# Kernel tuning notes

Hardware: AMD Instinct MI355X
Metric: run time of the kernel (lower is better)

The kernel has to match this reference:

```python
import jax, jax.numpy as jnp
import numpy as np

N_NODES = 50000
N_EDGES = 600000
D_IN = 128
D_OUT = 128


def mean_propagate(x, edge_index, num_nodes):
    # edge_index[0] = source nodes, edge_index[1] = destination nodes
    src, dst = edge_index[0], edge_index[1]
    gathered = x[src]                                   # [E, D]
    summed = jax.ops.segment_sum(gathered, dst, num_segments=num_nodes)  # [N, D]
    deg = jax.ops.segment_sum(jnp.ones((edge_index.shape[1],), dtype=x.dtype), dst,
                              num_segments=num_nodes)   # [N]
    deg = jnp.maximum(deg, 1.0)
    return summed / deg[:, None]


def setup_inputs() -> dict:
    key = jax.random.key(0)
    k1, k2, k3 = jax.random.split(key, 3)
    x = jax.random.normal(k1, (N_NODES, D_IN), dtype=jnp.float32)
    edge_index = jax.random.randint(k2, (2, N_EDGES), 0, N_NODES, dtype=jnp.int64)
    # nn.Linear(in_channels*3, out_channels): weight [out, 3*in], bias [out]
    W = jax.random.normal(k3, (D_OUT, 3 * D_IN), dtype=jnp.float32) / np.sqrt(3 * D_IN)
    b = jnp.zeros((D_OUT,), dtype=jnp.float32)
    return {"x": x, "edge_index": edge_index, "W": W, "b": b}


def reference(x, edge_index, W, b):
    n = x.shape[0]
    hop1 = mean_propagate(x, edge_index, n)
    hop2 = mean_propagate(hop1, edge_index, n)
    feats = jnp.concatenate([x, hop1, hop2], axis=-1)   # [N, 3*D]
    return feats @ W.T + b                              # [N, D_OUT]
```

## Files before the change

kernel.cpp:

```cpp
#include <hip/hip_runtime.h>

#define N_NODES 50000
#define N_EDGES 600000
#define D 128
#define K3 (3 * D)
#define NB_G 1563
#define NB_H 2344
#define NREP 8
#define NB 196
#define LDSROW 104

typedef __attribute__((ext_vector_type(8))) short short8;
typedef __attribute__((ext_vector_type(4))) float floatx4;
typedef __attribute__((ext_vector_type(8))) unsigned short ushort8;

static __device__ __forceinline__ unsigned short f2bf(float f) {
    unsigned u = __float_as_uint(f);
    u += 0x7fff + ((u >> 16) & 1);
    return (unsigned short)(u >> 16);
}
static __device__ __forceinline__ float bf2f(unsigned short s) {
    return __uint_as_float(((unsigned)s) << 16);
}
static __device__ __forceinline__ unsigned pack2(float a, float b) {
    return (unsigned)f2bf(a) | ((unsigned)f2bf(b) << 16);
}

__global__ __launch_bounds__(256) void prep_kernel(const float* __restrict__ x,
                                                   const float* __restrict__ W,
                                                   unsigned short* __restrict__ xb,
                                                   unsigned short* __restrict__ Wr,
                                                   int* __restrict__ counts8) {
    const int stride = gridDim.x * 256;
    const int t0 = blockIdx.x * 256 + threadIdx.x;
    for (int i = t0; i < NREP * N_NODES; i += stride) counts8[i] = 0;
    for (unsigned t = t0; t < (unsigned)N_NODES * 16; t += stride) {
        unsigned n = t >> 4;
        unsigned c = (t & 15u) << 3;
        const float4 v0 = *(const float4*)(x + (size_t)n * D + c);
        const float4 v1 = *(const float4*)(x + (size_t)n * D + c + 4);
        ushort8 o;
        o[0] = f2bf(v0.x); o[1] = f2bf(v0.y); o[2] = f2bf(v0.z); o[3] = f2bf(v0.w);
        o[4] = f2bf(v1.x); o[5] = f2bf(v1.y); o[6] = f2bf(v1.z); o[7] = f2bf(v1.w);
        *(ushort8*)(xb + (size_t)n * D + c) = o;
    }
    for (unsigned id = t0; id < 24u * 4u * 64u; id += stride) {
        unsigned T = id >> 8;
        unsigned ks = (id >> 6) & 3u;
        unsigned lane = id & 63u;
        unsigned c = lane & 15u;
        unsigned q = lane >> 4;
        unsigned row = (T & 7u) * 16u + c;
        unsigned k = (T >> 3) * 128u + ks * 32u + q * 8u;
        const float4 v0 = *(const float4*)(W + (size_t)row * K3 + k);
        const float4 v1 = *(const float4*)(W + (size_t)row * K3 + k + 4);
        ushort8 o;
        o[0] = f2bf(v0.x); o[1] = f2bf(v0.y); o[2] = f2bf(v0.z); o[3] = f2bf(v0.w);
        o[4] = f2bf(v1.x); o[5] = f2bf(v1.y); o[6] = f2bf(v1.z); o[7] = f2bf(v1.w);
        *(ushort8*)(Wr + (size_t)id * 8) = o;
    }
}

__global__ __launch_bounds__(256) void gemmhist_kernel(const unsigned short* __restrict__ xb,
                                                       const unsigned short* __restrict__ Wr,
                                                       const float* __restrict__ bias,
                                                       const int* __restrict__ dst,
                                                       unsigned short* __restrict__ z,
                                                       int* __restrict__ counts8) {
    __shared__ unsigned short lds[4 * 32 * LDSROW];
    const int blk = blockIdx.x;
    if (blk >= NB_G) {
        int e = (blk - NB_G) * 256 + threadIdx.x;
        if (e < N_EDGES) atomicAdd(&counts8[((e >> 2) & 7) * N_NODES + dst[e]], 1);
        return;
    }
    const int tid = threadIdx.x;
    const int wave = tid >> 6;
    const int lane = tid & 63;
    const int col = lane & 15;
    const int quad = lane >> 4;
    const int mbase = blk * 32;
    const int T0 = wave * 6;

    int r0 = mbase + col;
    int r1 = mbase + 16 + col;
    if (r0 >= N_NODES) r0 = N_NODES - 1;
    if (r1 >= N_NODES) r1 = N_NODES - 1;
    const unsigned short* ap0 = xb + (size_t)r0 * D + quad * 8;
    const unsigned short* ap1 = xb + (size_t)r1 * D + quad * 8;

    short8 a0r[4], a1r[4];
#pragma unroll
    for (int ks = 0; ks < 4; ++ks) {
        a0r[ks] = *(const short8*)(ap0 + ks * 32);
        a1r[ks] = *(const short8*)(ap1 + ks * 32);
    }
    short8 br[24];
#pragma unroll
    for (int t = 0; t < 6; ++t)
#pragma unroll
        for (int ks = 0; ks < 4; ++ks)
            br[t * 4 + ks] = *(const short8*)(Wr + (size_t)(((T0 + t) * 4 + ks) * 64 + lane) * 8);

    floatx4 acc0[6], acc1[6];
#pragma unroll
    for (int t = 0; t < 6; ++t) {
        acc0[t] = (floatx4){0.f, 0.f, 0.f, 0.f};
        acc1[t] = (floatx4){0.f, 0.f, 0.f, 0.f};
    }
#pragma unroll
    for (int ks = 0; ks < 4; ++ks) {
#pragma unroll
        for (int t = 0; t < 6; ++t) {
            acc0[t] = __builtin_amdgcn_mfma_f32_16x16x32_bf16(br[t * 4 + ks], a0r[ks], acc0[t], 0, 0, 0);
            acc1[t] = __builtin_amdgcn_mfma_f32_16x16x32_bf16(br[t * 4 + ks], a1r[ks], acc1[t], 0, 0, 0);
        }
    }

    unsigned short* wlds = lds + wave * 32 * LDSROW;
#pragma unroll
    for (int t = 0; t < 6; ++t) {
        int T = T0 + t;
        float4 bq = (float4){0.f, 0.f, 0.f, 0.f};
        if (T < 8) bq = *(const float4*)(bias + T * 16 + quad * 4);
        uint2 p;
        p.x = pack2(acc0[t][0] + bq.x, acc0[t][1] + bq.y);
        p.y = pack2(acc0[t][2] + bq.z, acc0[t][3] + bq.w);
        *(uint2*)(wlds + col * LDSROW + t * 16 + quad * 4) = p;
        uint2 q2;
        q2.x = pack2(acc1[t][0] + bq.x, acc1[t][1] + bq.y);
        q2.y = pack2(acc1[t][2] + bq.z, acc1[t][3] + bq.w);
        *(uint2*)(wlds + (col + 16) * LDSROW + t * 16 + quad * 4) = q2;
    }
    __syncthreads();
#pragma unroll
    for (int it = 0; it < 6; ++it) {
        int id = it * 64 + lane;
        int row = id / 12;
        int ch = id - row * 12;
        int node = mbase + row;
        ushort8 v = *(const ushort8*)(wlds + row * LDSROW + ch * 8);
        if (node < N_NODES)
            *(ushort8*)(z + (size_t)node * K3 + T0 * 16 + ch * 8) = v;
    }
}

__global__ __launch_bounds__(256) void bsum_kernel(const int* __restrict__ counts8,
                                                   int* __restrict__ ctot,
                                                   int* __restrict__ bsum) {
    __shared__ int wsum[4];
    int tid = threadIdx.x;
    int i = blockIdx.x * 256 + tid;
    int v = 0;
    if (i < N_NODES) {
#pragma unroll
        for (int r = 0; r < NREP; ++r) v += counts8[r * N_NODES + i];
        ctot[i] = v;
    }
#pragma unroll
    for (int d = 32; d >= 1; d >>= 1) v += __shfl_xor(v, d);
    if ((tid & 63) == 0) wsum[tid >> 6] = v;
    __syncthreads();
    if (tid == 0) bsum[blockIdx.x] = wsum[0] + wsum[1] + wsum[2] + wsum[3];
}

__global__ __launch_bounds__(256) void scan_bsum_kernel(const int* __restrict__ bsum,
                                                        int* __restrict__ bexcl,
                                                        int* __restrict__ off, int nb) {
    __shared__ int wsum[4];
    int tid = threadIdx.x;
    int lane = tid & 63, wid = tid >> 6;
    int v = (tid < nb) ? bsum[tid] : 0;
    int x = v;
#pragma unroll
    for (int d = 1; d < 64; d <<= 1) {
        int u = __shfl_up(x, d);
        if (lane >= d) x += u;
    }
    if (lane == 63) wsum[wid] = x;
    __syncthreads();
    int prefix = 0;
    for (int w = 0; w < wid; ++w) prefix += wsum[w];
    if (tid < nb) bexcl[tid] = prefix + x - v;
    if (tid == 0) off[N_NODES] = N_EDGES;
}

__global__ __launch_bounds__(256) void scan_final_kernel(const int* __restrict__ ctot,
                                                         const int* __restrict__ counts8,
                                                         const int* __restrict__ bexcl,
                                                         int* __restrict__ off,
                                                         int* __restrict__ cursor8) {
    __shared__ int wsum[4];
    int tid = threadIdx.x;
    int lane = tid & 63, wid = tid >> 6;
    int i = blockIdx.x * 256 + tid;
    int v = (i < N_NODES) ? ctot[i] : 0;
    int x = v;
#pragma unroll
    for (int d = 1; d < 64; d <<= 1) {
        int u = __shfl_up(x, d);
        if (lane >= d) x += u;
    }
    if (lane == 63) wsum[wid] = x;
    __syncthreads();
    int prefix = 0;
    for (int w = 0; w < wid; ++w) prefix += wsum[w];
    if (i < N_NODES) {
        int excl = bexcl[blockIdx.x] + prefix + x - v;
        off[i] = excl;
        int run = excl;
#pragma unroll
        for (int r = 0; r < NREP; ++r) {
            cursor8[r * N_NODES + i] = run;
            run += counts8[r * N_NODES + i];
        }
    }
}

__global__ __launch_bounds__(256) void fill_kernel(const int* __restrict__ src,
                                                   const int* __restrict__ dst,
                                                   int* __restrict__ cursor8,
                                                   int* __restrict__ csr_src) {
    int u = blockIdx.x * 256 + threadIdx.x;
    if (u < N_EDGES / 4) {
        int4 s4 = ((const int4*)src)[u];
        int4 d4 = ((const int4*)dst)[u];
        int* cbase = cursor8 + (u & 7) * N_NODES;
        csr_src[atomicAdd(cbase + d4.x, 1)] = s4.x;
        csr_src[atomicAdd(cbase + d4.y, 1)] = s4.y;
        csr_src[atomicAdd(cbase + d4.z, 1)] = s4.z;
        csr_src[atomicAdd(cbase + d4.w, 1)] = s4.w;
    }
}

__global__ __launch_bounds__(256) void gather1_kernel(const unsigned short* __restrict__ z,
                                                      const int* __restrict__ off,
                                                      const int* __restrict__ csr_src,
                                                      unsigned short* __restrict__ tb) {
    unsigned n = (blockIdx.x * 256 + threadIdx.x) >> 6;
    if (n >= N_NODES) return;
    const int lane = threadIdx.x & 63;
    const int s = lane >> 4;
    const unsigned c = (lane & 15u) << 3;
    const unsigned short* fin = z + 256 + c;
    const int2 ee = *(const int2*)(off + n);
    const int e0 = ee.x, e1 = ee.y;
    float acc[8] = {0.f, 0.f, 0.f, 0.f, 0.f, 0.f, 0.f, 0.f};
    for (int base = (e0 & ~3) + s * 4; base < e1; base += 16) {
        int4 idx = *(const int4*)(csr_src + base);
        float m0 = (base >= e0) ? 1.f : 0.f;
        float m1 = (base + 1 >= e0 && base + 1 < e1) ? 1.f : 0.f;
        float m2 = (base + 2 >= e0 && base + 2 < e1) ? 1.f : 0.f;
        float m3 = (base + 3 >= e0 && base + 3 < e1) ? 1.f : 0.f;
        int s0 = min(max(idx.x, 0), N_NODES - 1);
        int s1 = min(max(idx.y, 0), N_NODES - 1);
        int s2 = min(max(idx.z, 0), N_NODES - 1);
        int s3 = min(max(idx.w, 0), N_NODES - 1);
        ushort8 v0 = *(const ushort8*)(fin + (size_t)s0 * K3);
        ushort8 v1 = *(const ushort8*)(fin + (size_t)s1 * K3);
        ushort8 v2 = *(const ushort8*)(fin + (size_t)s2 * K3);
        ushort8 v3 = *(const ushort8*)(fin + (size_t)s3 * K3);
#pragma unroll
        for (int j = 0; j < 8; ++j)
            acc[j] += (m0 * bf2f(v0[j]) + m1 * bf2f(v1[j])) +
                      (m2 * bf2f(v2[j]) + m3 * bf2f(v3[j]));
    }
#pragma unroll
    for (int j = 0; j < 8; ++j) {
        acc[j] += __shfl_xor(acc[j], 16);
        acc[j] += __shfl_xor(acc[j], 32);
    }
    if (s == 0) {
        float inv = 1.0f / fmaxf((float)(e1 - e0), 1.0f);
        ushort8 za = *(const ushort8*)(z + (size_t)n * K3 + 128 + c);
        ushort8 o;
#pragma unroll
        for (int j = 0; j < 8; ++j) o[j] = f2bf(bf2f(za[j]) + acc[j] * inv);
        *(ushort8*)(tb + (size_t)n * D + c) = o;
    }
}

__global__ __launch_bounds__(256) void gather2_kernel(const unsigned short* __restrict__ z,
                                                      const unsigned short* __restrict__ tb,
                                                      const int* __restrict__ off,
                                                      const int* __restrict__ csr_src,
                                                      float* __restrict__ out) {
    unsigned n = (blockIdx.x * 256 + threadIdx.x) >> 6;
    if (n >= N_NODES) return;
    const int lane = threadIdx.x & 63;
    const int s = lane >> 4;
    const unsigned c = (lane & 15u) << 3;
    const unsigned short* fin = tb + c;
    const int2 ee = *(const int2*)(off + n);
    const int e0 = ee.x, e1 = ee.y;
    float acc[8] = {0.f, 0.f, 0.f, 0.f, 0.f, 0.f, 0.f, 0.f};
    for (int base = (e0 & ~3) + s * 4; base < e1; base += 16) {
        int4 idx = *(const int4*)(csr_src + base);
        float m0 = (base >= e0) ? 1.f : 0.f;
        float m1 = (base + 1 >= e0 && base + 1 < e1) ? 1.f : 0.f;
        float m2 = (base + 2 >= e0 && base + 2 < e1) ? 1.f : 0.f;
        float m3 = (base + 3 >= e0 && base + 3 < e1) ? 1.f : 0.f;
        int s0 = min(max(idx.x, 0), N_NODES - 1);
        int s1 = min(max(idx.y, 0), N_NODES - 1);
        int s2 = min(max(idx.z, 0), N_NODES - 1);
        int s3 = min(max(idx.w, 0), N_NODES - 1);
        ushort8 v0 = *(const ushort8*)(fin + (size_t)s0 * D);
        ushort8 v1 = *(const ushort8*)(fin + (size_t)s1 * D);
        ushort8 v2 = *(const ushort8*)(fin + (size_t)s2 * D);
        ushort8 v3 = *(const ushort8*)(fin + (size_t)s3 * D);
#pragma unroll
        for (int j = 0; j < 8; ++j)
            acc[j] += (m0 * bf2f(v0[j]) + m1 * bf2f(v1[j])) +
                      (m2 * bf2f(v2[j]) + m3 * bf2f(v3[j]));
    }
#pragma unroll
    for (int j = 0; j < 8; ++j) {
        acc[j] += __shfl_xor(acc[j], 16);
        acc[j] += __shfl_xor(acc[j], 32);
    }
    if (s == 0) {
        float inv = 1.0f / fmaxf((float)(e1 - e0), 1.0f);
        ushort8 za = *(const ushort8*)(z + (size_t)n * K3 + c);
        float4 q0, q1;
        q0.x = bf2f(za[0]) + acc[0] * inv;
        q0.y = bf2f(za[1]) + acc[1] * inv;
        q0.z = bf2f(za[2]) + acc[2] * inv;
        q0.w = bf2f(za[3]) + acc[3] * inv;
        q1.x = bf2f(za[4]) + acc[4] * inv;
        q1.y = bf2f(za[5]) + acc[5] * inv;
        q1.z = bf2f(za[6]) + acc[6] * inv;
        q1.w = bf2f(za[7]) + acc[7] * inv;
        *(float4*)(out + (size_t)n * D + c) = q0;
        *(float4*)(out + (size_t)n * D + c + 4) = q1;
    }
}

extern "C" void kernel_launch(void* const* d_in, const int* in_sizes, int n_in,
                              void* d_out, int out_size, void* d_ws, size_t ws_size,
                              hipStream_t stream) {
    const float* x = (const float*)d_in[0];
    const int* ei = (const int*)d_in[1];
    const float* W = (const float*)d_in[2];
    const float* b = (const float*)d_in[3];
    float* out = (float*)d_out;
    const int* src = ei;
    const int* dst = ei + N_EDGES;

    unsigned short* xb = (unsigned short*)d_ws;
    unsigned short* z = xb + (size_t)N_NODES * D;
    unsigned short* tb = z + (size_t)N_NODES * K3;
    unsigned short* Wr = tb + (size_t)N_NODES * D;
    int* counts8 = (int*)(Wr + 6144 * 8);
    int* ctot = counts8 + NREP * N_NODES;
    int* bsumv = ctot + N_NODES;
    int* bexclv = bsumv + 256;
    int* offv = bexclv + 256;
    int* cursor8v = offv + (N_NODES + 4);
    int* csrv = cursor8v + NREP * N_NODES;

    prep_kernel<<<800, 256, 0, stream>>>(x, W, xb, Wr, counts8);
    gemmhist_kernel<<<NB_G + NB_H, 256, 0, stream>>>(xb, Wr, b, dst, z, counts8);
    bsum_kernel<<<NB, 256, 0, stream>>>(counts8, ctot, bsumv);
    scan_bsum_kernel<<<1, 256, 0, stream>>>(bsumv, bexclv, offv, NB);
    scan_final_kernel<<<NB, 256, 0, stream>>>(ctot, counts8, bexclv, offv, cursor8v);
    fill_kernel<<<(N_EDGES / 4 + 255) / 256, 256, 0, stream>>>(src, dst, cursor8v, csrv);

    const int ggrid = (N_NODES * 64 + 255) / 256;
    gather1_kernel<<<ggrid, 256, 0, stream>>>(z, offv, csrv, tb);
    gather2_kernel<<<ggrid, 256, 0, stream>>>(z, tb, offv, csrv, out);
}
```

Measured before the change: 208.8 us.

## Replace CSR build with fixed-capacity per-node buckets plus overflow list

Removes the histogram, two scan kernels and the CSR fill. A single atomic pass now writes source indices into fixed 64-slot per-destination buckets, and edges beyond capacity go to a global overflow list. The gathers read from the buckets and scan the overflow list only for nodes whose degree exceeds the cap. The GEMM is split into its own kernel that processes four 32-row tiles per block so the weight registers are reused. This saves several launches and passes but adds uncontended-per-node atomics on a single counter array and a larger, sparser bucket buffer.

```diff
diff --git a/kernel.cpp b/kernel.cpp
--- a/kernel.cpp
+++ b/kernel.cpp
@@ -4,10 +4,9 @@
 #define N_EDGES 600000
 #define D 128
 #define K3 (3 * D)
-#define NB_G 1563
-#define NB_H 2344
-#define NREP 8
-#define NB 196
+#define CAP 64
+#define SM 4
+#define NB_G2 391
 #define LDSROW 104
 
 typedef __attribute__((ext_vector_type(8))) short short8;
@@ -30,10 +29,10 @@
                                                    const float* __restrict__ W,
                                                    unsigned short* __restrict__ xb,
                                                    unsigned short* __restrict__ Wr,
-                                                   int* __restrict__ counts8) {
+                                                   int* __restrict__ cnt) {
     const int stride = gridDim.x * 256;
     const int t0 = blockIdx.x * 256 + threadIdx.x;
-    for (int i = t0; i < NREP * N_NODES; i += stride) counts8[i] = 0;
+    for (int i = t0; i < N_NODES + 4; i += stride) cnt[i] = 0;
     for (unsigned t = t0; t < (unsigned)N_NODES * 16; t += stride) {
         unsigned n = t >> 4;
         unsigned c = (t & 15u) << 3;
@@ -61,40 +60,43 @@
     }
 }
 
-__global__ __launch_bounds__(256) void gemmhist_kernel(const unsigned short* __restrict__ xb,
-                                                       const unsigned short* __restrict__ Wr,
-                                                       const float* __restrict__ bias,
-                                                       const int* __restrict__ dst,
-                                                       unsigned short* __restrict__ z,
-                                                       int* __restrict__ counts8) {
+__global__ __launch_bounds__(256) void fillb_kernel(const int* __restrict__ src,
+                                                    const int* __restrict__ dst,
+                                                    int* __restrict__ cnt,
+                                                    int* __restrict__ bucket,
+                                                    int2* __restrict__ ovf) {
+    int* ovfcnt = cnt + N_NODES;
+    int u = blockIdx.x * 256 + threadIdx.x;
+    if (u < N_EDGES / 4) {
+        int4 s4 = ((const int4*)src)[u];
+        int4 d4 = ((const int4*)dst)[u];
+        int p0 = atomicAdd(&cnt[d4.x], 1);
+        if (p0 < CAP) bucket[(size_t)d4.x * CAP + p0] = s4.x;
+        else ovf[atomicAdd(ovfcnt, 1)] = make_int2(d4.x, s4.x);
+        int p1 = atomicAdd(&cnt[d4.y], 1);
+        if (p1 < CAP) bucket[(size_t)d4.y * CAP + p1] = s4.y;
+        else ovf[atomicAdd(ovfcnt, 1)] = make_int2(d4.y, s4.y);
+        int p2 = atomicAdd(&cnt[d4.z], 1);
+        if (p2 < CAP) bucket[(size_t)d4.z * CAP + p2] = s4.z;
+        else ovf[atomicAdd(ovfcnt, 1)] = make_int2(d4.z, s4.z);
+        int p3 = atomicAdd(&cnt[d4.w], 1);
+        if (p3 < CAP) bucket[(size_t)d4.w * CAP + p3] = s4.w;
+        else ovf[atomicAdd(ovfcnt, 1)] = make_int2(d4.w, s4.w);
+    }
+}
+
+__global__ __launch_bounds__(256) void gemm_kernel(const unsigned short* __restrict__ xb,
+                                                   const unsigned short* __restrict__ Wr,
+                                                   const float* __restrict__ bias,
+                                                   unsigned short* __restrict__ z) {
     __shared__ unsigned short lds[4 * 32 * LDSROW];
-    const int blk = blockIdx.x;
-    if (blk >= NB_G) {
-        int e = (blk - NB_G) * 256 + threadIdx.x;
-        if (e < N_EDGES) atomicAdd(&counts8[((e >> 2) & 7) * N_NODES + dst[e]], 1);
-        return;
-    }
     const int tid = threadIdx.x;
     const int wave = tid >> 6;
     const int lane = tid & 63;
     const int col = lane & 15;
     const int quad = lane >> 4;
-    const int mbase = blk * 32;
     const int T0 = wave * 6;
 
-    int r0 = mbase + col;
-    int r1 = mbase + 16 + col;
-    if (r0 >= N_NODES) r0 = N_NODES - 1;
-    if (r1 >= N_NODES) r1 = N_NODES - 1;
-    const unsigned short* ap0 = xb + (size_t)r0 * D + quad * 8;
-    const unsigned short* ap1 = xb + (size_t)r1 * D + quad * 8;
-
-    short8 a0r[4], a1r[4];
-#pragma unroll
-    for (int ks = 0; ks < 4; ++ks) {
-        a0r[ks] = *(const short8*)(ap0 + ks * 32);
-        a1r[ks] = *(const short8*)(ap1 + ks * 32);
-    }
     short8 br[24];
 #pragma unroll
     for (int t = 0; t < 6; ++t)
@@ -102,140 +104,75 @@
         for (int ks = 0; ks < 4; ++ks)
             br[t * 4 + ks] = *(const short8*)(Wr + (size_t)(((T0 + t) * 4 + ks) * 64 + lane) * 8);
 
-    floatx4 acc0[6], acc1[6];
-#pragma unroll
-    for (int t = 0; t < 6; ++t) {
-        acc0[t] = (floatx4){0.f, 0.f, 0.f, 0.f};
-        acc1[t] = (floatx4){0.f, 0.f, 0.f, 0.f};
-    }
-#pragma unroll
-    for (int ks = 0; ks < 4; ++ks) {
+    float4 bq = (float4){0.f, 0.f, 0.f, 0.f};
+
+    unsigned short* wlds = lds + wave * 32 * LDSROW;
+
+    for (int sidx = 0; sidx < SM; ++sidx) {
+        const int mbase = blockIdx.x * (SM * 32) + sidx * 32;
+        int r0 = mbase + col;
+        int r1 = mbase + 16 + col;
+        if (r0 >= N_NODES) r0 = N_NODES - 1;
+        if (r1 >= N_NODES) r1 = N_NODES - 1;
+        const unsigned short* ap0 = xb + (size_t)r0 * D + quad * 8;
+        const unsigned short* ap1 = xb + (size_t)r1 * D + quad * 8;
+        short8 a0r[4], a1r[4];
+#pragma unroll
+        for (int ks = 0; ks < 4; ++ks) {
+            a0r[ks] = *(const short8*)(ap0 + ks * 32);
+            a1r[ks] = *(const short8*)(ap1 + ks * 32);
+        }
+
+        floatx4 acc0[6], acc1[6];
 #pragma unroll
         for (int t = 0; t < 6; ++t) {
-            acc0[t] = __builtin_amdgcn_mfma_f32_16x16x32_bf16(br[t * 4 + ks], a0r[ks], acc0[t], 0, 0, 0);
-            acc1[t] = __builtin_amdgcn_mfma_f32_16x16x32_bf16(br[t * 4 + ks], a1r[ks], acc1[t], 0, 0, 0);
-        }
-    }
-
-    unsigned short* wlds = lds + wave * 32 * LDSROW;
-#pragma unroll
-    for (int t = 0; t < 6; ++t) {
-        int T = T0 + t;
-        float4 bq = (float4){0.f, 0.f, 0.f, 0.f};
-        if (T < 8) bq = *(const float4*)(bias + T * 16 + quad * 4);
-        uint2 p;
-        p.x = pack2(acc0[t][0] + bq.x, acc0[t][1] + bq.y);
-        p.y = pack2(acc0[t][2] + bq.z, acc0[t][3] + bq.w);
-        *(uint2*)(wlds + col * LDSROW + t * 16 + quad * 4) = p;
-        uint2 q2;
-        q2.x = pack2(acc1[t][0] + bq.x, acc1[t][1] + bq.y);
-        q2.y = pack2(acc1[t][2] + bq.z, acc1[t][3] + bq.w);
-        *(uint2*)(wlds + (col + 16) * LDSROW + t * 16 + quad * 4) = q2;
-    }
-    __syncthreads();
-#pragma unroll
-    for (int it = 0; it < 6; ++it) {
-        int id = it * 64 + lane;
-        int row = id / 12;
-        int ch = id - row * 12;
-        int node = mbase + row;
-        ushort8 v = *(const ushort8*)(wlds + row * LDSROW + ch * 8);
-        if (node < N_NODES)
-            *(ushort8*)(z + (size_t)node * K3 + T0 * 16 + ch * 8) = v;
-    }
-}
-
-__global__ __launch_bounds__(256) void bsum_kernel(const int* __restrict__ counts8,
-                                                   int* __restrict__ ctot,
-                                                   int* __restrict__ bsum) {
-    __shared__ int wsum[4];
-    int tid = threadIdx.x;
-    int i = blockIdx.x * 256 + tid;
-    int v = 0;
-    if (i < N_NODES) {
-#pragma unroll
-        for (int r = 0; r < NREP; ++r) v += counts8[r * N_NODES + i];
-        ctot[i] = v;
-    }
-#pragma unroll
-    for (int d = 32; d >= 1; d >>= 1) v += __shfl_xor(v, d);
-    if ((tid & 63) == 0) wsum[tid >> 6] = v;
-    __syncthreads();
-    if (tid == 0) bsum[blockIdx.x] = wsum[0] + wsum[1] + wsum[2] + wsum[3];
-}
-
-__global__ __launch_bounds__(256) void scan_bsum_kernel(const int* __restrict__ bsum,
-                                                        int* __restrict__ bexcl,
-                                                        int* __restrict__ off, int nb) {
-    __shared__ int wsum[4];
-    int tid = threadIdx.x;
-    int lane = tid & 63, wid = tid >> 6;
-    int v = (tid < nb) ? bsum[tid] : 0;
-    int x = v;
-#pragma unroll
-    for (int d = 1; d < 64; d <<= 1) {
-        int u = __shfl_up(x, d);
-        if (lane >= d) x += u;
-    }
-    if (lane == 63) wsum[wid] = x;
-    __syncthreads();
-    int prefix = 0;
-    for (int w = 0; w < wid; ++w) prefix += wsum[w];
-    if (tid < nb) bexcl[tid] = prefix + x - v;
-    if (tid == 0) off[N_NODES] = N_EDGES;
-}
-
-__global__ __launch_bounds__(256) void scan_final_kernel(const int* __restrict__ ctot,
-                                                         const int* __restrict__ counts8,
-                                                         const int* __restrict__ bexcl,
-                                                         int* __restrict__ off,
-                                                         int* __restrict__ cursor8) {
-    __shared__ int wsum[4];
-    int tid = threadIdx.x;
-    int lane = tid & 63, wid = tid >> 6;
-    int i = blockIdx.x * 256 + tid;
-    int v = (i < N_NODES) ? ctot[i] : 0;
-    int x = v;
-#pragma unroll
-    for (int d = 1; d < 64; d <<= 1) {
-        int u = __shfl_up(x, d);
-        if (lane >= d) x += u;
-    }
-    if (lane == 63) wsum[wid] = x;
-    __syncthreads();
-    int prefix = 0;
-    for (int w = 0; w < wid; ++w) prefix += wsum[w];
-    if (i < N_NODES) {
-        int excl = bexcl[blockIdx.x] + prefix + x - v;
-        off[i] = excl;
-        int run = excl;
-#pragma unroll
-        for (int r = 0; r < NREP; ++r) {
-            cursor8[r * N_NODES + i] = run;
-            run += counts8[r * N_NODES + i];
-        }
-    }
-}
-
-__global__ __launch_bounds__(256) void fill_kernel(const int* __restrict__ src,
-                                                   const int* __restrict__ dst,
-                                                   int* __restrict__ cursor8,
-                                                   int* __restrict__ csr_src) {
-    int u = blockIdx.x * 256 + threadIdx.x;
-    if (u < N_EDGES / 4) {
-        int4 s4 = ((const int4*)src)[u];
-        int4 d4 = ((const int4*)dst)[u];
-        int* cbase = cursor8 + (u & 7) * N_NODES;
-        csr_src[atomicAdd(cbase + d4.x, 1)] = s4.x;
-        csr_src[atomicAdd(cbase + d4.y, 1)] = s4.y;
-        csr_src[atomicAdd(cbase + d4.z, 1)] = s4.z;
-        csr_src[atomicAdd(cbase + d4.w, 1)] = s4.w;
+            acc0[t] = (floatx4){0.f, 0.f, 0.f, 0.f};
+            acc1[t] = (floatx4){0.f, 0.f, 0.f, 0.f};
+        }
+#pragma unroll
+        for (int ks = 0; ks < 4; ++ks) {
+#pragma unroll
+            for (int t = 0; t < 6; ++t) {
+                acc0[t] = __builtin_amdgcn_mfma_f32_16x16x32_bf16(br[t * 4 + ks], a0r[ks], acc0[t], 0, 0, 0);
+                acc1[t] = __builtin_amdgcn_mfma_f32_16x16x32_bf16(br[t * 4 + ks], a1r[ks], acc1[t], 0, 0, 0);
+            }
+        }
+
+#pragma unroll
+        for (int t = 0; t < 6; ++t) {
+            int T = T0 + t;
+            bq = (float4){0.f, 0.f, 0.f, 0.f};
+            if (T < 8) bq = *(const float4*)(bias + T * 16 + quad * 4);
+            uint2 p;
+            p.x = pack2(acc0[t][0] + bq.x, acc0[t][1] + bq.y);
+            p.y = pack2(acc0[t][2] + bq.z, acc0[t][3] + bq.w);
+            *(uint2*)(wlds + col * LDSROW + t * 16 + quad * 4) = p;
+            uint2 q2;
+            q2.x = pack2(acc1[t][0] + bq.x, acc1[t][1] + bq.y);
+            q2.y = pack2(acc1[t][2] + bq.z, acc1[t][3] + bq.w);
+            *(uint2*)(wlds + (col + 16) * LDSROW + t * 16 + quad * 4) = q2;
+        }
+        __syncthreads();
+#pragma unroll
+        for (int it = 0; it < 6; ++it) {
+            int id = it * 256 + tid;
+            int row = id / 48;
+            int ch = id - row * 48;
+            int w = ch / 12;
+            int cc = (ch - w * 12) * 8;
+            int node = mbase + row;
+            ushort8 v = *(const ushort8*)(lds + (size_t)w * 32 * LDSROW + row * LDSROW + cc);
+            if (node < N_NODES)
+                *(ushort8*)(z + (size_t)node * K3 + ch * 8) = v;
+        }
+        __syncthreads();
     }
 }
 
 __global__ __launch_bounds__(256) void gather1_kernel(const unsigned short* __restrict__ z,
-                                                      const int* __restrict__ off,
-                                                      const int* __restrict__ csr_src,
+                                                      const int* __restrict__ cnt,
+                                                      const int* __restrict__ bucket,
+                                                      const int2* __restrict__ ovf,
                                                       unsigned short* __restrict__ tb) {
     unsigned n = (blockIdx.x * 256 + threadIdx.x) >> 6;
     if (n >= N_NODES) return;
@@ -243,15 +180,16 @@
     const int s = lane >> 4;
     const unsigned c = (lane & 15u) << 3;
     const unsigned short* fin = z + 256 + c;
-    const int2 ee = *(const int2*)(off + n);
-    const int e0 = ee.x, e1 = ee.y;
+    const int deg = cnt[n];
+    const int dcap = min(deg, CAP);
+    const int* bp = bucket + (size_t)n * CAP;
     float acc[8] = {0.f, 0.f, 0.f, 0.f, 0.f, 0.f, 0.f, 0.f};
-    for (int base = (e0 & ~3) + s * 4; base < e1; base += 16) {
-        int4 idx = *(const int4*)(csr_src + base);
-        float m0 = (base >= e0) ? 1.f : 0.f;
-        float m1 = (base + 1 >= e0 && base + 1 < e1) ? 1.f : 0.f;
-        float m2 = (base + 2 >= e0 && base + 2 < e1) ? 1.f : 0.f;
-        float m3 = (base + 3 >= e0 && base + 3 < e1) ? 1.f : 0.f;
+    for (int base = s * 4; base < dcap; base += 16) {
+        int4 idx = *(const int4*)(bp + base);
+        float m0 = 1.f;
+        float m1 = (base + 1 < dcap) ? 1.f : 0.f;
+        float m2 = (base + 2 < dcap) ? 1.f : 0.f;
+        float m3 = (base + 3 < dcap) ? 1.f : 0.f;
         int s0 = min(max(idx.x, 0), N_NODES - 1);
         int s1 = min(max(idx.y, 0), N_NODES - 1);
         int s2 = min(max(idx.z, 0), N_NODES - 1);
@@ -265,13 +203,25 @@
             acc[j] += (m0 * bf2f(v0[j]) + m1 * bf2f(v1[j])) +
                       (m2 * bf2f(v2[j]) + m3 * bf2f(v3[j]));
     }
+    if (deg > CAP) {
+        int oc = cnt[N_NODES];
+        if (s == 0)
+            for (int i = 0; i < oc; ++i) {
+                int2 p = ovf[i];
+                if (p.x == (int)n) {
+                    ushort8 v = *(const ushort8*)(fin + (size_t)p.y * K3);
+#pragma unroll
+                    for (int j = 0; j < 8; ++j) acc[j] += bf2f(v[j]);
+                }
+            }
+    }
 #pragma unroll
     for (int j = 0; j < 8; ++j) {
         acc[j] += __shfl_xor(acc[j], 16);
         acc[j] += __shfl_xor(acc[j], 32);
     }
     if (s == 0) {
-        float inv = 1.0f / fmaxf((float)(e1 - e0), 1.0f);
+        float inv = 1.0f / fmaxf((float)deg, 1.0f);
         ushort8 za = *(const ushort8*)(z + (size_t)n * K3 + 128 + c);
         ushort8 o;
 #pragma unroll
@@ -282,8 +232,9 @@
 
 __global__ __launch_bounds__(256) void gather2_kernel(const unsigned short* __restrict__ z,
                                                       const unsigned short* __restrict__ tb,
-                                                      const int* __restrict__ off,
-                                                      const int* __restrict__ csr_src,
+                                                      const int* __restrict__ cnt,
+                                                      const int* __restrict__ bucket,
+                                                      const int2* __restrict__ ovf,
                                                       float* __restrict__ out) {
     unsigned n = (blockIdx.x * 256 + threadIdx.x) >> 6;
     if (n >= N_NODES) return;
@@ -291,15 +242,16 @@
     const int s = lane >> 4;
     const unsigned c = (lane & 15u) << 3;
     const unsigned short* fin = tb + c;
-    const int2 ee = *(const int2*)(off + n);
-    const int e0 = ee.x, e1 = ee.y;
+    const int deg = cnt[n];
+    const int dcap = min(deg, CAP);
+    const int* bp = bucket + (size_t)n * CAP;
     float acc[8] = {0.f, 0.f, 0.f, 0.f, 0.f, 0.f, 0.f, 0.f};
-    for (int base = (e0 & ~3) + s * 4; base < e1; base += 16) {
-        int4 idx = *(const int4*)(csr_src + base);
-        float m0 = (base >= e0) ? 1.f : 0.f;
-        float m1 = (base + 1 >= e0 && base + 1 < e1) ? 1.f : 0.f;
-        float m2 = (base + 2 >= e0 && base + 2 < e1) ? 1.f : 0.f;
-        float m3 = (base + 3 >= e0 && base + 3 < e1) ? 1.f : 0.f;
+    for (int base = s * 4; base < dcap; base += 16) {
+        int4 idx = *(const int4*)(bp + base);
+        float m0 = 1.f;
+        float m1 = (base + 1 < dcap) ? 1.f : 0.f;
+        float m2 = (base + 2 < dcap) ? 1.f : 0.f;
+        float m3 = (base + 3 < dcap) ? 1.f : 0.f;
         int s0 = min(max(idx.x, 0), N_NODES - 1);
         int s1 = min(max(idx.y, 0), N_NODES - 1);
         int s2 = min(max(idx.z, 0), N_NODES - 1);
@@ -313,13 +265,25 @@
             acc[j] += (m0 * bf2f(v0[j]) + m1 * bf2f(v1[j])) +
                       (m2 * bf2f(v2[j]) + m3 * bf2f(v3[j]));
     }
+    if (deg > CAP) {
+        int oc = cnt[N_NODES];
+        if (s == 0)
+            for (int i = 0; i < oc; ++i) {
+                int2 p = ovf[i];
+                if (p.x == (int)n) {
+                    ushort8 v = *(const ushort8*)(fin + (size_t)p.y * D);
+#pragma unroll
+                    for (int j = 0; j < 8; ++j) acc[j] += bf2f(v[j]);
+                }
+            }
+    }
 #pragma unroll
     for (int j = 0; j < 8; ++j) {
         acc[j] += __shfl_xor(acc[j], 16);
         acc[j] += __shfl_xor(acc[j], 32);
     }
     if (s == 0) {
-        float inv = 1.0f / fmaxf((float)(e1 - e0), 1.0f);
+        float inv = 1.0f / fmaxf((float)deg, 1.0f);
         ushort8 za = *(const ushort8*)(z + (size_t)n * K3 + c);
         float4 q0, q1;
         q0.x = bf2f(za[0]) + acc[0] * inv;
@@ -350,22 +314,15 @@
     unsigned short* z = xb + (size_t)N_NODES * D;
     unsigned short* tb = z + (size_t)N_NODES * K3;
     unsigned short* Wr = tb + (size_t)N_NODES * D;
-    int* counts8 = (int*)(Wr + 6144 * 8);
-    int* ctot = counts8 + NREP * N_NODES;
-    int* bsumv = ctot + N_NODES;
-    int* bexclv = bsumv + 256;
-    int* offv = bexclv + 256;
-    int* cursor8v = offv + (N_NODES + 4);
-    int* csrv = cursor8v + NREP * N_NODES;
-
-    prep_kernel<<<800, 256, 0, stream>>>(x, W, xb, Wr, counts8);
-    gemmhist_kernel<<<NB_G + NB_H, 256, 0, stream>>>(xb, Wr, b, dst, z, counts8);
-    bsum_kernel<<<NB, 256, 0, stream>>>(counts8, ctot, bsumv);
-    scan_bsum_kernel<<<1, 256, 0, stream>>>(bsumv, bexclv, offv, NB);
-    scan_final_kernel<<<NB, 256, 0, stream>>>(ctot, counts8, bexclv, offv, cursor8v);
-    fill_kernel<<<(N_EDGES / 4 + 255) / 256, 256, 0, stream>>>(src, dst, cursor8v, csrv);
+    int* cnt = (int*)(Wr + 6144 * 8);
+    int* bucket = cnt + N_NODES + 4;
+    int2* ovf = (int2*)(bucket + (size_t)N_NODES * CAP);
+
+    prep_kernel<<<800, 256, 0, stream>>>(x, W, xb, Wr, cnt);
+    fillb_kernel<<<(N_EDGES / 4 + 255) / 256, 256, 0, stream>>>(src, dst, cnt, bucket, ovf);
+    gemm_kernel<<<NB_G2, 256, 0, stream>>>(xb, Wr, b, z);
 
     const int ggrid = (N_NODES * 64 + 255) / 256;
-    gather1_kernel<<<ggrid, 256, 0, stream>>>(z, offv, csrv, tb);
-    gather2_kernel<<<ggrid, 256, 0, stream>>>(z, tb, offv, csrv, out);
-}
+    gather1_kernel<<<ggrid, 256, 0, stream>>>(z, cnt, bucket, ovf, tb);
+    gather2_kernel<<<ggrid, 256, 0, stream>>>(z, tb, cnt, bucket, ovf, out);
+}
```

After: 188.5 us. 9.7% less time.
